# Optimization experiments

Measured on AMD Instinct MI355X. Metric: run time of the kernel, lower is better.

The kernel has to match this reference:

```python
import jax, jax.numpy as jnp
import numpy as np

KH = KW = 3
PAD = 1


def _conv2d(x, w, b):
    y = jax.lax.conv_general_dilated(
        x, w, window_strides=(1, 1), padding=((PAD, PAD), (PAD, PAD)),
        dimension_numbers=("NCHW", "OIHW", "NCHW"))
    return y + b[None, :, None, None]


def _bilinear_sample_one(img, ys, xs):
    # img: [C,H,W]; ys,xs: [K,h,w] absolute sampling coords; zeros outside.
    C, H, W = img.shape
    flat = img.reshape(C, H * W)
    y0 = jnp.floor(ys)
    x0 = jnp.floor(xs)
    wy = ys - y0
    wx = xs - x0

    def gather(yi, xi):
        valid = (yi >= 0) & (yi <= H - 1) & (xi >= 0) & (xi <= W - 1)
        yc = jnp.clip(yi, 0, H - 1).astype(jnp.int32)
        xc = jnp.clip(xi, 0, W - 1).astype(jnp.int32)
        idx = (yc * W + xc).reshape(-1)
        v = jnp.take(flat, idx, axis=1).reshape((C,) + yi.shape)
        return v * valid.astype(img.dtype)

    v00 = gather(y0, x0)
    v01 = gather(y0, x0 + 1)
    v10 = gather(y0 + 1, x0)
    v11 = gather(y0 + 1, x0 + 1)
    return (v00 * (1 - wy) * (1 - wx) + v01 * (1 - wy) * wx
            + v10 * wy * (1 - wx) + v11 * wy * wx)  # [C,K,h,w]


def deform_conv2d(x, offset, weight, bias):
    # x: [B,C,H,W]; offset: [B,2K,h,w] with (dy,dx) per tap; stride 1, pad 1.
    B, C, H, W = x.shape
    h, w = offset.shape[2], offset.shape[3]
    K = KH * KW
    off = offset.reshape(B, K, 2, h, w)
    ky = (jnp.arange(K) // KW - PAD).astype(x.dtype)  # tap row displacement
    kx = (jnp.arange(K) % KW - PAD).astype(x.dtype)
    ii = jnp.arange(h, dtype=x.dtype)[None, :, None]
    jj = jnp.arange(w, dtype=x.dtype)[None, None, :]
    ys = ii - PAD + ky[:, None, None] + off[:, :, 0]  # [B,K,h,w]
    xs = jj - PAD + kx[:, None, None] + off[:, :, 1]
    sampled = jax.vmap(_bilinear_sample_one)(x, ys, xs)  # [B,C,K,h,w]
    Co = weight.shape[0]
    out = jnp.einsum('ock,bckhw->bohw', weight.reshape(Co, C, K), sampled)
    return out + bias[None, :, None, None]


def setup_inputs() -> dict:
    key = jax.random.key(0)
    ks = jax.random.split(key, 5)
    B, C, H, W = 4, 64, 128, 128
    x = jax.random.normal(ks[0], (B, C, H, W), dtype=jnp.float32)
    w_off = jax.random.normal(ks[1], (4, C, KH, KW), dtype=jnp.float32) * 0.05
    b_off = jnp.zeros((4,), dtype=jnp.float32)
    weight = jax.random.normal(ks[2], (C, C, KH, KW), dtype=jnp.float32) * 0.05
    bias = jnp.zeros((C,), dtype=jnp.float32)
    # base_offset: canonical 3x3 tap displacements, layout (dy,dx) per tap.
    ky = np.repeat(np.arange(KH) - PAD, KW).astype(np.float32)
    kx = np.tile(np.arange(KW) - PAD, KH).astype(np.float32)
    base = np.stack([ky, kx], axis=1).reshape(-1)  # [18]
    base_offset = jnp.asarray(np.broadcast_to(base[None, :, None, None], (1, 18, H, W)).copy())
    idx = np.arange(18)
    mask1 = jnp.asarray(idx % 2 == 0)  # y coords -> scale1
    mask2 = jnp.asarray(idx % 2 == 1)  # x coords -> scale2
    return {"x": x, "w_off": w_off, "b_off": b_off, "weight": weight,
            "bias": bias, "base_offset": base_offset, "mask1": mask1, "mask2": mask2}


def reference(x, w_off, b_off, weight, bias, base_offset, mask1, mask2):
    off = _conv2d(x, w_off, b_off)  # [B,4,h,w]
    scale1 = jax.nn.relu(off[:, 2:3]) + 1.0  # [B,1,h,w]
    scale2 = jax.nn.relu(off[:, 3:4]) + 1.0
    shift = jnp.tile(off[:, :2], (1, KH * KW, 1, 1))  # [B,18,h,w]
    # scaled_offset[:, mask1] = base*scale1 ; scaled_offset[:, mask2] = base*scale2
    scale_full = jnp.where(mask1[None, :, None, None], scale1, scale2)  # [B,18,h,w]
    offset = base_offset * scale_full - base_offset + shift
    return deform_conv2d(x, offset, weight, bias)
```

## Files before the change

kernel.cpp:

```cpp
#include <hip/hip_runtime.h>

#define Hd 128
#define Wd 128
#define Cd 64
#define COd 64
#define Bd 4
#define HWd (Hd*Wd)

typedef __attribute__((ext_vector_type(8))) _Float16 half8;
typedef __attribute__((ext_vector_type(2))) _Float16 h2;
typedef __attribute__((ext_vector_type(4))) float    f32x4;

__device__ __align__(16) _Float16 g_wh[COd*576];
__device__ __align__(16) _Float16 g_woffh[16*576];
__device__ float4 g_offs[Bd*HWd];
__device__ __align__(16) unsigned short g_xt[(size_t)Bd*HWd*Cd];

static __device__ __forceinline__ unsigned cvtpkh(float lo, float hi) {
    unsigned r;
    asm("v_cvt_pkrtz_f16_f32 %0, %1, %2" : "=v"(r) : "v"(lo), "v"(hi));
    return r;
}
static __device__ __forceinline__ h2 ash2(unsigned u) {
    union { unsigned u; h2 h; } x; x.u = u; return x.h;
}
static __device__ __forceinline__ unsigned ash2u(h2 h) {
    union { h2 h; unsigned u; } x; x.h = h; return x.u;
}

__global__ __launch_bounds__(256) void k_prep(const float* __restrict__ x,
                                              const float* __restrict__ weight,
                                              const float* __restrict__ w_off) {
    int bid = blockIdx.x;
    if (bid < 512) {
        int b = bid >> 7, y = bid & 127;
        int px = threadIdx.x & 127;
        int h  = threadIdx.x >> 7;
        const float* xb = x + (size_t)b*Cd*HWd + y*Wd + px;
        unsigned short* ob = g_xt + ((size_t)(b*HWd) + y*Wd + px)*Cd + h*32;
        #pragma unroll
        for (int oct = 0; oct < 4; ++oct) {
            unsigned pk[4];
            #pragma unroll
            for (int e = 0; e < 4; ++e) {
                float v0 = xb[(size_t)(h*32 + oct*8 + 2*e    )*HWd];
                float v1 = xb[(size_t)(h*32 + oct*8 + 2*e + 1)*HWd];
                pk[e] = cvtpkh(v0, v1);
            }
            *(uint4*)(ob + oct*8) = make_uint4(pk[0], pk[1], pk[2], pk[3]);
        }
    } else if (bid < 656) {
        int g = (bid - 512)*256 + threadIdx.x;
        if (g < COd*576) {
            int co = g / 576, k = g % 576;
            int t = k >> 6, c = k & 63;
            g_wh[g] = (_Float16)weight[(co*Cd + c)*9 + t];
        }
    } else {
        int g = (bid - 656)*256 + threadIdx.x;
        if (g < 16*576) {
            int row = g / 576, k = g % 576;
            int t = k >> 6, c = k & 63;
            g_woffh[g] = (row < 4) ? (_Float16)w_off[(row*Cd + c)*9 + t] : (_Float16)0.f;
        }
    }
}

__global__ __launch_bounds__(256) void k_offs(const float* __restrict__ b_off) {
    __shared__ uint4 lds_x[3*8*128];
    int orig = blockIdx.x;
    int xcd = orig & 7, slot = orig >> 3;
    int g = xcd*2 + (slot >> 5);
    int b = g >> 2;
    int i = (g & 3)*32 + (slot & 31);

    int tid = threadIdx.x;
    const unsigned short* xb = g_xt + (size_t)b*HWd*Cd;

    #pragma unroll
    for (int rr = 0; rr < 3; ++rr) {
        int y = i + rr - 1;
        bool rv = (y >= 0) && (y <= 127);
        #pragma unroll
        for (int k = 0; k < 4; ++k) {
            int n = k*256 + tid;
            int px = n >> 3, c = n & 7;
            uint4 v = rv ? *(const uint4*)(xb + (size_t)(y*Wd + px)*Cd + c*8)
                         : make_uint4(0, 0, 0, 0);
            lds_x[(rr*8 + c)*128 + px] = v;
        }
    }
    __syncthreads();

    int w = tid >> 6, l = tid & 63;
    int pc = l & 15, q = l >> 4;
    const _Float16* arow = g_woffh + pc*576 + q*8;
    float bo0 = b_off[0], bo1 = b_off[1], bo2 = b_off[2], bo3 = b_off[3];

    #pragma unroll
    for (int tile = 0; tile < 2; ++tile) {
        int j = (w*2 + tile)*16 + pc;
        f32x4 acc = {0.f, 0.f, 0.f, 0.f};
        #pragma unroll
        for (int t = 0; t < 9; ++t) {
            int dy = t/3, dx = t%3 - 1;
            int px = j + dx;
            bool ok = (px >= 0) && (px <= 127);
            int pxc = min(max(px, 0), 127);
            uint4 u0 = lds_x[(dy*8 + q    )*128 + pxc];
            uint4 u1 = lds_x[(dy*8 + q + 4)*128 + pxc];
            if (!ok) { u0 = make_uint4(0,0,0,0); u1 = make_uint4(0,0,0,0); }
            half8 a0 = *(const half8*)(arow + (2*t    )*32);
            half8 a1 = *(const half8*)(arow + (2*t + 1)*32);
            acc = __builtin_amdgcn_mfma_f32_16x16x32_f16(a0, *(half8*)&u0, acc, 0, 0, 0);
            acc = __builtin_amdgcn_mfma_f32_16x16x32_f16(a1, *(half8*)&u1, acc, 0, 0, 0);
        }
        if (q == 0) {
            float o0 = acc[0] + bo0;
            float o1 = acc[1] + bo1;
            float o2 = fmaxf(acc[2] + bo2, 0.f) + 1.f;
            float o3 = fmaxf(acc[3] + bo3, 0.f) + 1.f;
            g_offs[(b*Hd + i)*Wd + j] = make_float4(o0, o1, o2, o3);
        }
    }
}

#define GATHER(T, U00, U01, U10, U11, H00, H01, H10, H11)                         \
    {                                                                             \
        float ys = (float)(i - 1) + (float)((T)/3 - 1)*s1v + off0;                \
        float xs = (float)(jA - 1) + (float)((T)%3 - 1)*s2v + off1;               \
        float y0f = floorf(ys), x0f = floorf(xs);                                 \
        float wy = ys - y0f, wx = xs - x0f;                                       \
        float vy0 = (y0f >=  0.f && y0f <= 127.f) ? 1.f : 0.f;                    \
        float vy1 = (y0f >= -1.f && y0f <= 126.f) ? 1.f : 0.f;                    \
        float vx0 = (x0f >=  0.f && x0f <= 127.f) ? 1.f : 0.f;                    \
        float vx1 = (x0f >= -1.f && x0f <= 126.f) ? 1.f : 0.f;                    \
        float w00 = (1.f-wy)*(1.f-wx)*vy0*vx0, w01 = (1.f-wy)*wx*vy0*vx1;         \
        float w10 = wy*(1.f-wx)*vy1*vx0,       w11 = wy*wx*vy1*vx1;               \
        H00 = ash2(cvtpkh(w00, w00)); H01 = ash2(cvtpkh(w01, w01));               \
        H10 = ash2(cvtpkh(w10, w10)); H11 = ash2(cvtpkh(w11, w11));               \
        int iy0 = min(max((int)y0f,     0), 127), iy1 = min(max((int)y0f+1,0),127);\
        int ix0 = min(max((int)x0f,     0), 127), ix1 = min(max((int)x0f+1,0),127);\
        U00 = *(const uint4*)(xb + (size_t)(iy0*Wd + ix0)*Cd + oct*8);            \
        U01 = *(const uint4*)(xb + (size_t)(iy0*Wd + ix1)*Cd + oct*8);            \
        U10 = *(const uint4*)(xb + (size_t)(iy1*Wd + ix0)*Cd + oct*8);            \
        U11 = *(const uint4*)(xb + (size_t)(iy1*Wd + ix1)*Cd + oct*8);            \
    }

#define PACK_STORE(BUF, U00, U01, U10, U11, H00, H01, H10, H11)                   \
    {                                                                             \
        unsigned a00[4] = {U00.x,U00.y,U00.z,U00.w};                              \
        unsigned a01[4] = {U01.x,U01.y,U01.z,U01.w};                              \
        unsigned a10[4] = {U10.x,U10.y,U10.z,U10.w};                              \
        unsigned a11[4] = {U11.x,U11.y,U11.z,U11.w};                              \
        unsigned pk[4];                                                           \
        _Pragma("unroll")                                                         \
        for (int e = 0; e < 4; ++e) {                                             \
            h2 r = ash2(a00[e])*H00 + ash2(a01[e])*H01                            \
                 + ash2(a10[e])*H10 + ash2(a11[e])*H11;                           \
            pk[e] = ash2u(r);                                                     \
        }                                                                         \
        lds_b[(((BUF)*2 + par)*2 + nt)*64 + slotA] = make_uint4(pk[0],pk[1],pk[2],pk[3]); \
    }

__global__ __launch_bounds__(256) void k_deform(const float* __restrict__ bias,
                                                float* __restrict__ out) {
    __shared__ uint4 lds_b[2*2*2*64];
    int orig = blockIdx.x;
    int xcd = orig & 7, slotB = orig >> 3;
    int g = xcd*2 + (slotB >> 7);
    int s = slotB & 127;
    int b = g >> 2;
    int i = (g & 3)*32 + (s >> 2);
    int j0 = (s & 3) << 5;

    int w = threadIdx.x >> 6, l = threadIdx.x & 63;
    int oct = l & 7, px8 = l >> 3;
    int pxl = w*8 + px8;
    int jA  = j0 + pxl;
    int nt = pxl >> 4, pcA = pxl & 15, qA = oct & 3, par = oct >> 2;
    int slotA = (pcA ^ (qA << 1)) + (qA << 4);
    int pcB = l & 15, qB = l >> 4;
    int physl = (pcB ^ (qB << 1)) + (qB << 4);
    const _Float16* wrow = g_wh + (size_t)(w*16 + pcB)*576 + qB*8;

    const unsigned short* xb = g_xt + (size_t)b*HWd*Cd;
    float4 o4 = g_offs[(b*Hd + i)*Wd + jA];
    float off0 = o4.x, off1 = o4.y, s1v = o4.z, s2v = o4.w;

    f32x4 acc0 = {0.f,0.f,0.f,0.f};
    f32x4 acc1 = {0.f,0.f,0.f,0.f};

    uint4 gc00, gc01, gc10, gc11, gn00, gn01, gn10, gn11;
    h2 hc00, hc01, hc10, hc11, hn00, hn01, hn10, hn11;

    GATHER(0, gc00, gc01, gc10, gc11, hc00, hc01, hc10, hc11);

    #pragma unroll
    for (int t = 0; t < 9; ++t) {
        if (t < 8) {
            GATHER(t+1, gn00, gn01, gn10, gn11, hn00, hn01, hn10, hn11);
        }
        PACK_STORE(t & 1, gc00, gc01, gc10, gc11, hc00, hc01, hc10, hc11);
        __syncthreads();
        {
            half8 a0 = *(const half8*)(wrow + (2*t    )*32);
            half8 a1 = *(const half8*)(wrow + (2*t + 1)*32);
            half8 b00 = *(const half8*)&lds_b[(((t&1)*2 + 0)*2 + 0)*64 + physl];
            half8 b01 = *(const half8*)&lds_b[(((t&1)*2 + 0)*2 + 1)*64 + physl];
            half8 b10 = *(const half8*)&lds_b[(((t&1)*2 + 1)*2 + 0)*64 + physl];
            half8 b11 = *(const half8*)&lds_b[(((t&1)*2 + 1)*2 + 1)*64 + physl];
            acc0 = __builtin_amdgcn_mfma_f32_16x16x32_f16(a0, b00, acc0, 0, 0, 0);
            acc1 = __builtin_amdgcn_mfma_f32_16x16x32_f16(a0, b01, acc1, 0, 0, 0);
            acc0 = __builtin_amdgcn_mfma_f32_16x16x32_f16(a1, b10, acc0, 0, 0, 0);
            acc1 = __builtin_amdgcn_mfma_f32_16x16x32_f16(a1, b11, acc1, 0, 0, 0);
        }
        if (t < 8) {
            gc00 = gn00; gc01 = gn01; gc10 = gn10; gc11 = gn11;
            hc00 = hn00; hc01 = hn01; hc10 = hn10; hc11 = hn11;
        }
    }

    #pragma unroll
    for (int rr = 0; rr < 4; ++rr) {
        int co = w*16 + qB*4 + rr;
        float bco = bias[co];
        size_t base = ((size_t)(b*COd + co)*Hd + i)*Wd + j0;
        out[base + pcB]      = acc0[rr] + bco;
        out[base + 16 + pcB] = acc1[rr] + bco;
    }
}

extern "C" void kernel_launch(void* const* d_in, const int* in_sizes, int n_in,
                              void* d_out, int out_size, void* d_ws, size_t ws_size,
                              hipStream_t stream) {
    const float* x      = (const float*)d_in[0];
    const float* w_off  = (const float*)d_in[1];
    const float* b_off  = (const float*)d_in[2];
    const float* weight = (const float*)d_in[3];
    const float* bias   = (const float*)d_in[4];
    float* out = (float*)d_out;

    hipLaunchKernelGGL(k_prep,   dim3(692),  dim3(256), 0, stream, x, weight, w_off);
    hipLaunchKernelGGL(k_offs,   dim3(512),  dim3(256), 0, stream, b_off);
    hipLaunchKernelGGL(k_deform, dim3(2048), dim3(256), 0, stream, bias, out);
}
```

Measured before the change: 51.83 us.

## Halve deform block tile to 16 pixels with 2 waves covering 32 channels each

```diff
diff --git a/kernel.cpp b/kernel.cpp
--- a/kernel.cpp
+++ b/kernel.cpp
@@ -160,29 +160,31 @@
                  + ash2(a10[e])*H10 + ash2(a11[e])*H11;                           \
             pk[e] = ash2u(r);                                                     \
         }                                                                         \
-        lds_b[(((BUF)*2 + par)*2 + nt)*64 + slotA] = make_uint4(pk[0],pk[1],pk[2],pk[3]); \
-    }
-
-__global__ __launch_bounds__(256) void k_deform(const float* __restrict__ bias,
-                                                float* __restrict__ out) {
-    __shared__ uint4 lds_b[2*2*2*64];
+        lds_b[((BUF)*2 + par)*64 + slotA] = make_uint4(pk[0], pk[1], pk[2], pk[3]); \
+    }
+
+__global__ __launch_bounds__(128, 8) void k_deform(const float* __restrict__ bias,
+                                                   float* __restrict__ out) {
+    __shared__ uint4 lds_b[2*2*64];
     int orig = blockIdx.x;
     int xcd = orig & 7, slotB = orig >> 3;
-    int g = xcd*2 + (slotB >> 7);
-    int s = slotB & 127;
+    int g = xcd*2 + (slotB >> 8);
+    int s = slotB & 255;
     int b = g >> 2;
-    int i = (g & 3)*32 + (s >> 2);
-    int j0 = (s & 3) << 5;
-
-    int w = threadIdx.x >> 6, l = threadIdx.x & 63;
-    int oct = l & 7, px8 = l >> 3;
-    int pxl = w*8 + px8;
+    int i = (g & 3)*32 + (s >> 3);
+    int j0 = (s & 7) << 4;
+
+    int tid = threadIdx.x;
+    int w = tid >> 6, l = tid & 63;
+    int oct = tid & 7;
+    int pxl = tid >> 3;
     int jA  = j0 + pxl;
-    int nt = pxl >> 4, pcA = pxl & 15, qA = oct & 3, par = oct >> 2;
+    int pcA = pxl, qA = oct & 3, par = oct >> 2;
     int slotA = (pcA ^ (qA << 1)) + (qA << 4);
     int pcB = l & 15, qB = l >> 4;
     int physl = (pcB ^ (qB << 1)) + (qB << 4);
-    const _Float16* wrow = g_wh + (size_t)(w*16 + pcB)*576 + qB*8;
+    const _Float16* wrow0 = g_wh + (size_t)(w*32 + pcB)*576 + qB*8;
+    const _Float16* wrow1 = wrow0 + (size_t)16*576;
 
     const unsigned short* xb = g_xt + (size_t)b*HWd*Cd;
     float4 o4 = g_offs[(b*Hd + i)*Wd + jA];
@@ -204,16 +206,16 @@
         PACK_STORE(t & 1, gc00, gc01, gc10, gc11, hc00, hc01, hc10, hc11);
         __syncthreads();
         {
-            half8 a0 = *(const half8*)(wrow + (2*t    )*32);
-            half8 a1 = *(const half8*)(wrow + (2*t + 1)*32);
-            half8 b00 = *(const half8*)&lds_b[(((t&1)*2 + 0)*2 + 0)*64 + physl];
-            half8 b01 = *(const half8*)&lds_b[(((t&1)*2 + 0)*2 + 1)*64 + physl];
-            half8 b10 = *(const half8*)&lds_b[(((t&1)*2 + 1)*2 + 0)*64 + physl];
-            half8 b11 = *(const half8*)&lds_b[(((t&1)*2 + 1)*2 + 1)*64 + physl];
-            acc0 = __builtin_amdgcn_mfma_f32_16x16x32_f16(a0, b00, acc0, 0, 0, 0);
-            acc1 = __builtin_amdgcn_mfma_f32_16x16x32_f16(a0, b01, acc1, 0, 0, 0);
-            acc0 = __builtin_amdgcn_mfma_f32_16x16x32_f16(a1, b10, acc0, 0, 0, 0);
-            acc1 = __builtin_amdgcn_mfma_f32_16x16x32_f16(a1, b11, acc1, 0, 0, 0);
+            half8 a00 = *(const half8*)(wrow0 + (2*t    )*32);
+            half8 a01 = *(const half8*)(wrow0 + (2*t + 1)*32);
+            half8 a10 = *(const half8*)(wrow1 + (2*t    )*32);
+            half8 a11 = *(const half8*)(wrow1 + (2*t + 1)*32);
+            half8 be = *(const half8*)&lds_b[((t&1)*2 + 0)*64 + physl];
+            half8 bo = *(const half8*)&lds_b[((t&1)*2 + 1)*64 + physl];
+            acc0 = __builtin_amdgcn_mfma_f32_16x16x32_f16(a00, be, acc0, 0, 0, 0);
+            acc0 = __builtin_amdgcn_mfma_f32_16x16x32_f16(a01, bo, acc0, 0, 0, 0);
+            acc1 = __builtin_amdgcn_mfma_f32_16x16x32_f16(a10, be, acc1, 0, 0, 0);
+            acc1 = __builtin_amdgcn_mfma_f32_16x16x32_f16(a11, bo, acc1, 0, 0, 0);
         }
         if (t < 8) {
             gc00 = gn00; gc01 = gn01; gc10 = gn10; gc11 = gn11;
@@ -223,11 +225,10 @@
 
     #pragma unroll
     for (int rr = 0; rr < 4; ++rr) {
-        int co = w*16 + qB*4 + rr;
-        float bco = bias[co];
-        size_t base = ((size_t)(b*COd + co)*Hd + i)*Wd + j0;
-        out[base + pcB]      = acc0[rr] + bco;
-        out[base + 16 + pcB] = acc1[rr] + bco;
+        int co0 = w*32 + qB*4 + rr;
+        int co1 = co0 + 16;
+        out[((size_t)(b*COd + co0)*Hd + i)*Wd + j0 + pcB] = acc0[rr] + bias[co0];
+        out[((size_t)(b*COd + co1)*Hd + i)*Wd + j0 + pcB] = acc1[rr] + bias[co1];
     }
 }
 
@@ -243,5 +244,5 @@
 
     hipLaunchKernelGGL(k_prep,   dim3(692),  dim3(256), 0, stream, x, weight, w_off);
     hipLaunchKernelGGL(k_offs,   dim3(512),  dim3(256), 0, stream, b_off);
-    hipLaunchKernelGGL(k_deform, dim3(2048), dim3(256), 0, stream, bias, out);
-}
+    hipLaunchKernelGGL(k_deform, dim3(4096), dim3(128), 0, stream, bias, out);
+}
```

After: 67.14 us. 1.3x slower.
